# Kernel optimization log

Measured on AMD Instinct MI355X. Metric: run time of the kernel, lower is better.

## Reference

```python
import jax, jax.numpy as jnp
import numpy as np


def setup_inputs() -> dict:
    key = jax.random.key(0)
    k1, k2, k3, k4 = jax.random.split(key, 4)
    B, M, N = 8, 4096, 4096
    return {
        "pc_src": jax.random.normal(k1, (B, 3, M), dtype=jnp.float32),
        "pc_dst": jax.random.normal(k2, (B, 3, N), dtype=jnp.float32),
        "sigma_src": jax.random.uniform(k3, (B, M), dtype=jnp.float32),
        "sigma_dst": jax.random.uniform(k4, (B, N), dtype=jnp.float32),
    }


def reference(pc_src, pc_dst, sigma_src, sigma_dst):
    # Pairwise Euclidean distance: diff[b, m, n] = ||pc_src[b,:,m] - pc_dst[b,:,n]||_2
    d = pc_src[:, :, :, None] - pc_dst[:, :, None, :]  # [B, 3, M, N]
    diff = jnp.sqrt(jnp.sum(d * d, axis=1))            # [B, M, N]

    # src -> dst
    src_dst_min_dist = jnp.min(diff, axis=2)           # [B, M]
    src_dst_I = jnp.argmin(diff, axis=2)               # [B, M]
    selected_sigma_dst = jnp.take_along_axis(sigma_dst, src_dst_I, axis=1)
    sigma_src_dst = (sigma_src + selected_sigma_dst) / 2
    forward_loss = jnp.mean(src_dst_min_dist * sigma_src_dst)

    # dst -> src
    dst_src_min_dist = jnp.min(diff, axis=1)           # [B, N]
    dst_src_I = jnp.argmin(diff, axis=1)               # [B, N]
    selected_sigma_src = jnp.take_along_axis(sigma_src, dst_src_I, axis=1)
    sigma_dst_src = (sigma_dst + selected_sigma_src) / 2
    backward_loss = jnp.mean(dst_src_min_dist * sigma_dst_src)

    return forward_loss + backward_loss
```

## Files before the change

### kernel.cpp

```cpp
#include <hip/hip_runtime.h>
#include <math.h>
#include <cfloat>

#define BLOCK 256
#define QPT 8
#define CS  64

typedef float f32x2 __attribute__((ext_vector_type(2)));
typedef float f32x4 __attribute__((ext_vector_type(4)));
typedef unsigned long long u64;

__global__ __launch_bounds__(BLOCK, 4)
void chamfer_min_kernel(const float* __restrict__ pc_src,
                        const float* __restrict__ pc_dst,
                        u64* __restrict__ part,
                        int M, int N, int B, int Zn) {
    __shared__ f32x4 lds4[CS];

    const int b = blockIdx.y;
    const int z = blockIdx.z;
    const int dir = (z >= Zn) ? 1 : 0;
    const int chunk = dir ? (z - Zn) : z;

    const int NQ = dir ? N : M;
    const int NR = dir ? M : N;
    const float* pcq = dir ? pc_dst : pc_src;
    const float* pcr = dir ? pc_src : pc_dst;
    u64* pp = part + (dir ? (size_t)B * M : (size_t)0) + (size_t)b * NQ;

    const int n0 = chunk * CS;
    const int tid = threadIdx.x;

    const float* rbase = pcr + (size_t)b * 3 * NR + n0;
    if (tid < CS / 2) {
        const int p = tid;
        const f32x2 rx = *(const f32x2*)(rbase + 2 * p);
        const f32x2 ry = *(const f32x2*)(rbase + NR + 2 * p);
        const f32x2 rz = *(const f32x2*)(rbase + 2 * NR + 2 * p);
        f32x4 w0, w1;
        w0.x = -2.0f * rx.x; w0.y = -2.0f * rx.y;
        w0.z = -2.0f * ry.x; w0.w = -2.0f * ry.y;
        w1.x = -2.0f * rz.x; w1.y = -2.0f * rz.y;
        w1.z = fmaf(rx.x, rx.x, fmaf(ry.x, ry.x, rz.x * rz.x)) + 64.0f;
        w1.w = fmaf(rx.y, rx.y, fmaf(ry.y, ry.y, rz.y * rz.y)) + 64.0f;
        lds4[2 * p]     = w0;
        lds4[2 * p + 1] = w1;
    }

    const int q0 = blockIdx.x * (BLOCK * QPT) + tid;
    const float* qb = pcq + (size_t)b * 3 * NQ;
    float qx[QPT], qy[QPT], qz[QPT];
    unsigned kmin[QPT];
#pragma unroll
    for (int j = 0; j < QPT; ++j) {
        const int q = q0 + j * BLOCK;
        qx[j] = qb[q];
        qy[j] = qb[NQ + q];
        qz[j] = qb[2 * NQ + q];
        kmin[j] = 0xFFFFFFFFu;
    }

    __syncthreads();

    const unsigned mask = ~(unsigned)(CS - 1);
#pragma unroll
    for (int p = 0; p < CS / 2; ++p) {
        const f32x4 w0 = lds4[2 * p];
        const f32x4 w1 = lds4[2 * p + 1];
#pragma unroll
        for (int j = 0; j < QPT; ++j) {
            float e0, e1;
            asm("v_fma_f32 %1, %5, %10, %12\n\t"
                "v_fma_f32 %2, %5, %11, %13\n\t"
                "v_fma_f32 %1, %4, %8, %1\n\t"
                "v_fma_f32 %2, %4, %9, %2\n\t"
                "v_fma_f32 %1, %3, %6, %1\n\t"
                "v_fma_f32 %2, %3, %7, %2\n\t"
                "v_and_or_b32 %1, %1, %14, %15\n\t"
                "v_and_or_b32 %2, %2, %14, %16\n\t"
                "v_min3_u32 %0, %1, %2, %0"
                : "+v"(kmin[j]), "=&v"(e0), "=&v"(e1)
                : "v"(qx[j]), "v"(qy[j]), "v"(qz[j]),
                  "v"(w0.x), "v"(w0.y), "v"(w0.z), "v"(w0.w),
                  "v"(w1.x), "v"(w1.y), "v"(w1.z), "v"(w1.w),
                  "s"(mask), "i"(2 * p), "i"(2 * p + 1));
        }
    }

#pragma unroll
    for (int j = 0; j < QPT; ++j) {
        const int q = q0 + j * BLOCK;
        const unsigned gidx = (unsigned)n0 + (kmin[j] & (unsigned)(CS - 1));
        const u64 key = ((u64)(kmin[j] & mask) << 32) | (u64)gidx;
        atomicMin(&pp[q], key);
    }
}

__global__ void chamfer_reduce_kernel(const float* __restrict__ pc_src,
                                      const float* __restrict__ pc_dst,
                                      const float* __restrict__ sig_src,
                                      const float* __restrict__ sig_dst,
                                      const u64* __restrict__ part,
                                      float* __restrict__ out,
                                      int M, int N, int B) {
    __shared__ float red[BLOCK];
    const int TT = blockIdx.x * BLOCK + threadIdx.x;
    const int dir = (TT >= B * M);
    const int t = dir ? TT - B * M : TT;

    const int NQ = dir ? N : M;
    const int NR = dir ? M : N;
    const float* pcq  = dir ? pc_dst : pc_src;
    const float* pcr  = dir ? pc_src : pc_dst;
    const float* sigq = dir ? sig_dst : sig_src;
    const float* sigr = dir ? sig_src : sig_dst;
    const float scale = 1.0f / (float)(B * NQ);

    const int b = t / NQ;
    const int q = t - b * NQ;

    const int gidx = (int)(unsigned)part[TT];

    const float* qbase = pcq + (size_t)b * 3 * NQ;
    const float* rbase = pcr + (size_t)b * 3 * NR;
    const float dx = qbase[q]          - rbase[gidx];
    const float dy = qbase[NQ + q]     - rbase[NR + gidx];
    const float dz = qbase[2 * NQ + q] - rbase[2 * NR + gidx];
    const float dist = sqrtf(fmaf(dx, dx, fmaf(dy, dy, dz * dz)));

    const float s = 0.5f * (sigq[t] + sigr[(size_t)b * NR + gidx]);
    red[threadIdx.x] = dist * s * scale;
    __syncthreads();

    for (int w = BLOCK / 2; w > 0; w >>= 1) {
        if (threadIdx.x < w) red[threadIdx.x] += red[threadIdx.x + w];
        __syncthreads();
    }
    if (threadIdx.x == 0) atomicAdd(out, red[0]);
}

extern "C" void kernel_launch(void* const* d_in, const int* in_sizes, int n_in,
                              void* d_out, int out_size, void* d_ws, size_t ws_size,
                              hipStream_t stream) {
    const float* pc_src  = (const float*)d_in[0];
    const float* pc_dst  = (const float*)d_in[1];
    const float* sig_src = (const float*)d_in[2];
    const float* sig_dst = (const float*)d_in[3];
    float* out = (float*)d_out;

    const int B = 8;
    const int M = in_sizes[2] / B;
    const int N = in_sizes[3] / B;
    const int NMAX = (M > N) ? M : N;

    const int Zn = N / CS;
    const int Zm = M / CS;

    u64* part = (u64*)d_ws;
    const size_t partBytes = (size_t)B * (M + N) * sizeof(u64);

    hipMemsetAsync(part, 0xFF, partBytes, stream);
    hipMemsetAsync(d_out, 0, sizeof(float), stream);

    {
        dim3 grid(NMAX / (BLOCK * QPT), B, Zn + Zm);
        chamfer_min_kernel<<<grid, BLOCK, 0, stream>>>(
            pc_src, pc_dst, part, M, N, B, Zn);
    }
    {
        dim3 rgrid((B * (M + N)) / BLOCK);
        chamfer_reduce_kernel<<<rgrid, BLOCK, 0, stream>>>(
            pc_src, pc_dst, sig_src, sig_dst, part, out, M, N, B);
    }
}
```

Measured before the change: 49.55 us.

## Compute pairwise distance keys with fp16 MFMA and wave-shuffle argmin reduction

Replaces the VALU FMA distance loop with 32x32x16 fp16 MFMA tiles. Query coordinates form the A fragment, and -2x reference coordinates the B fragment. The accumulator is seeded with each reference point's squared norm plus an offset. Per-lane min keys pack the masked float bits with a tile index. A cross-lane shuffle reduction then recovers the column before the atomicMin. Reference chunks grow to 2048 points per block, and the reduce kernel masks the index. This cuts per-pair VALU work, but fp16 coordinates can change argmin picks on near-ties, and most of the MFMA K dimension is zero padding.

```diff
diff --git a/kernel.cpp b/kernel.cpp
--- a/kernel.cpp
+++ b/kernel.cpp
@@ -1,26 +1,39 @@
 #include <hip/hip_runtime.h>
 #include <math.h>
-#include <cfloat>
 
 #define BLOCK 256
-#define QPT 8
-#define CS  64
+#define CN    2048
+#define NT    (CN / 32)
 
-typedef float f32x2 __attribute__((ext_vector_type(2)));
-typedef float f32x4 __attribute__((ext_vector_type(4)));
+typedef _Float16 f16;
+typedef _Float16 f16x8 __attribute__((ext_vector_type(8)));
+typedef float f32x16 __attribute__((ext_vector_type(16)));
 typedef unsigned long long u64;
 
+union HU { f16 h; unsigned short u; };
+static __device__ __forceinline__ unsigned short h16(float x) {
+    HU v; v.h = (f16)x; return v.u;
+}
+static __device__ __forceinline__ u64 shflxor32_u64(u64 v, int m) {
+    unsigned lo = (unsigned)v, hi = (unsigned)(v >> 32);
+    lo = __shfl_xor(lo, m, 32);
+    hi = __shfl_xor(hi, m, 32);
+    return ((u64)hi << 32) | lo;
+}
+
 __global__ __launch_bounds__(BLOCK, 4)
-void chamfer_min_kernel(const float* __restrict__ pc_src,
-                        const float* __restrict__ pc_dst,
-                        u64* __restrict__ part,
-                        int M, int N, int B, int Zn) {
-    __shared__ f32x4 lds4[CS];
+void chamfer_mfma_kernel(const float* __restrict__ pc_src,
+                         const float* __restrict__ pc_dst,
+                         u64* __restrict__ part,
+                         int M, int N, int B, int Zc0) {
+    __shared__ uint4 lds_ref[CN + 1];
+    __shared__ float lds_w[CN];
 
-    const int b = blockIdx.y;
-    const int z = blockIdx.z;
-    const int dir = (z >= Zn) ? 1 : 0;
-    const int chunk = dir ? (z - Zn) : z;
+    const int rg = blockIdx.x;
+    const int b  = blockIdx.y;
+    const int z  = blockIdx.z;
+    const int dir = (z >= Zc0) ? 1 : 0;
+    const int chunk = dir ? (z - Zc0) : z;
 
     const int NQ = dir ? N : M;
     const int NR = dir ? M : N;
@@ -28,71 +41,72 @@
     const float* pcr = dir ? pc_src : pc_dst;
     u64* pp = part + (dir ? (size_t)B * M : (size_t)0) + (size_t)b * NQ;
 
-    const int n0 = chunk * CS;
     const int tid = threadIdx.x;
+    const int lane = tid & 63;
+    const int wid = tid >> 6;
+    const int n0 = chunk * CN;
 
-    const float* rbase = pcr + (size_t)b * 3 * NR + n0;
-    if (tid < CS / 2) {
-        const int p = tid;
-        const f32x2 rx = *(const f32x2*)(rbase + 2 * p);
-        const f32x2 ry = *(const f32x2*)(rbase + NR + 2 * p);
-        const f32x2 rz = *(const f32x2*)(rbase + 2 * NR + 2 * p);
-        f32x4 w0, w1;
-        w0.x = -2.0f * rx.x; w0.y = -2.0f * rx.y;
-        w0.z = -2.0f * ry.x; w0.w = -2.0f * ry.y;
-        w1.x = -2.0f * rz.x; w1.y = -2.0f * rz.y;
-        w1.z = fmaf(rx.x, rx.x, fmaf(ry.x, ry.x, rz.x * rz.x)) + 64.0f;
-        w1.w = fmaf(rx.y, rx.y, fmaf(ry.y, ry.y, rz.y * rz.y)) + 64.0f;
-        lds4[2 * p]     = w0;
-        lds4[2 * p + 1] = w1;
+    const float* rb = pcr + (size_t)b * 3 * NR + n0;
+    for (int i = tid; i < CN; i += BLOCK) {
+        const float rx = rb[i], ry = rb[NR + i], rz = rb[2 * NR + i];
+        const unsigned u0 = (unsigned)h16(-2.0f * rx) | ((unsigned)h16(-2.0f * ry) << 16);
+        const unsigned u1 = (unsigned)h16(-2.0f * rz);
+        lds_ref[i] = make_uint4(u0, u1, 0u, 0u);
+        lds_w[i] = fmaf(rx, rx, fmaf(ry, ry, rz * rz)) + 64.0f;
     }
+    if (tid == 0) lds_ref[CN] = make_uint4(0u, 0u, 0u, 0u);
 
-    const int q0 = blockIdx.x * (BLOCK * QPT) + tid;
-    const float* qb = pcq + (size_t)b * 3 * NQ;
-    float qx[QPT], qy[QPT], qz[QPT];
-    unsigned kmin[QPT];
-#pragma unroll
-    for (int j = 0; j < QPT; ++j) {
-        const int q = q0 + j * BLOCK;
-        qx[j] = qb[q];
-        qy[j] = qb[NQ + q];
-        qz[j] = qb[2 * NQ + q];
-        kmin[j] = 0xFFFFFFFFu;
+    const int row0 = rg * 128 + wid * 32;
+    f16x8 afrag = {0, 0, 0, 0, 0, 0, 0, 0};
+    if (lane < 32) {
+        const float* qb = pcq + (size_t)b * 3 * NQ + row0 + lane;
+        afrag[0] = (f16)qb[0];
+        afrag[1] = (f16)qb[NQ];
+        afrag[2] = (f16)qb[2 * NQ];
     }
 
     __syncthreads();
 
-    const unsigned mask = ~(unsigned)(CS - 1);
+    const int col = lane & 31;
+    const bool lo = (lane < 32);
+    const uint4* bptr = lo ? &lds_ref[col] : &lds_ref[CN];
+    const int bstep = lo ? 32 : 0;
+
+    unsigned kmin[16];
 #pragma unroll
-    for (int p = 0; p < CS / 2; ++p) {
-        const f32x4 w0 = lds4[2 * p];
-        const f32x4 w1 = lds4[2 * p + 1];
+    for (int r = 0; r < 16; ++r) kmin[r] = 0xFFFFFFFFu;
+
+    const unsigned emask = ~127u;
+    const unsigned tj0 = (unsigned)(chunk * NT);
+
+    for (int t = 0; t < NT; ++t) {
+        const f16x8 bfrag = *(const f16x8*)bptr;
+        bptr += bstep;
+        const float wval = lds_w[t * 32 + col];
+        f32x16 acc;
 #pragma unroll
-        for (int j = 0; j < QPT; ++j) {
-            float e0, e1;
-            asm("v_fma_f32 %1, %5, %10, %12\n\t"
-                "v_fma_f32 %2, %5, %11, %13\n\t"
-                "v_fma_f32 %1, %4, %8, %1\n\t"
-                "v_fma_f32 %2, %4, %9, %2\n\t"
-                "v_fma_f32 %1, %3, %6, %1\n\t"
-                "v_fma_f32 %2, %3, %7, %2\n\t"
-                "v_and_or_b32 %1, %1, %14, %15\n\t"
-                "v_and_or_b32 %2, %2, %14, %16\n\t"
-                "v_min3_u32 %0, %1, %2, %0"
-                : "+v"(kmin[j]), "=&v"(e0), "=&v"(e1)
-                : "v"(qx[j]), "v"(qy[j]), "v"(qz[j]),
-                  "v"(w0.x), "v"(w0.y), "v"(w0.z), "v"(w0.w),
-                  "v"(w1.x), "v"(w1.y), "v"(w1.z), "v"(w1.w),
-                  "s"(mask), "i"(2 * p), "i"(2 * p + 1));
+        for (int r = 0; r < 16; ++r) acc[r] = wval;
+        acc = __builtin_amdgcn_mfma_f32_32x32x16_f16(afrag, bfrag, acc, 0, 0, 0);
+        const unsigned tj = tj0 + (unsigned)t;
+#pragma unroll
+        for (int r = 0; r < 16; ++r) {
+            const unsigned key = (__float_as_uint(acc[r]) & emask) | tj;
+            kmin[r] = key < kmin[r] ? key : kmin[r];
         }
     }
 
+    const int rhalf = (lane >> 5) * 4;
 #pragma unroll
-    for (int j = 0; j < QPT; ++j) {
-        const int q = q0 + j * BLOCK;
-        const unsigned gidx = (unsigned)n0 + (kmin[j] & (unsigned)(CS - 1));
-        const u64 key = ((u64)(kmin[j] & mask) << 32) | (u64)gidx;
-        atomicMin(&pp[q], key);
+    for (int r = 0; r < 16; ++r) {
+        u64 k64 = ((u64)kmin[r] << 5) | (unsigned)col;
+        for (int m2 = 1; m2 <= 16; m2 <<= 1) {
+            const u64 o = shflxor32_u64(k64, m2);
+            k64 = (o < k64) ? o : k64;
+        }
+        if (col == 0) {
+            const int row = (r & 3) + 8 * (r >> 2) + rhalf;
+            atomicMin(&pp[row0 + row], k64);
+        }
     }
 }
 
@@ -119,7 +133,7 @@
     const int b = t / NQ;
     const int q = t - b * NQ;
 
-    const int gidx = (int)(unsigned)part[TT];
+    const int gidx = (int)((unsigned)part[TT] & (unsigned)(NR - 1));
 
     const float* qbase = pcq + (size_t)b * 3 * NQ;
     const float* rbase = pcr + (size_t)b * 3 * NR;
@@ -151,10 +165,6 @@
     const int B = 8;
     const int M = in_sizes[2] / B;
     const int N = in_sizes[3] / B;
-    const int NMAX = (M > N) ? M : N;
-
-    const int Zn = N / CS;
-    const int Zm = M / CS;
 
     u64* part = (u64*)d_ws;
     const size_t partBytes = (size_t)B * (M + N) * sizeof(u64);
@@ -162,10 +172,13 @@
     hipMemsetAsync(part, 0xFF, partBytes, stream);
     hipMemsetAsync(d_out, 0, sizeof(float), stream);
 
+    const int Zc0 = N / CN;
+    const int Zc1 = M / CN;
+
     {
-        dim3 grid(NMAX / (BLOCK * QPT), B, Zn + Zm);
-        chamfer_min_kernel<<<grid, BLOCK, 0, stream>>>(
-            pc_src, pc_dst, part, M, N, B, Zn);
+        dim3 grid(M / 128, B, Zc0 + Zc1);
+        chamfer_mfma_kernel<<<grid, BLOCK, 0, stream>>>(
+            pc_src, pc_dst, part, M, N, B, Zc0);
     }
     {
         dim3 rgrid((B * (M + N)) / BLOCK);
```

Result: slower. 56.87 us (+14.8%).

## Precompute packed reference points in setup kernel and read them directly from global

Applied to the files above, without the earlier changes.

Adds a setup kernel that packs each reference point into a uint4 (-2x, -2y, -2z, |r|^2+64), initializes the partial-min buffer, and zeroes the output, replacing the two memsets. The min kernel drops its LDS staging and barrier, reads the packed points straight from global memory (uniform, so cached), and swaps the inline asm for plain C key/min code. It also raises launch bounds to 8 waves. The aim is less per-block setup and sync overhead plus higher occupancy. The risks are one extra launch, and compiler code that may be less tight than the hand-written min3/and_or sequence.

```diff
diff --git a/kernel.cpp b/kernel.cpp
--- a/kernel.cpp
+++ b/kernel.cpp
@@ -1,54 +1,59 @@
 #include <hip/hip_runtime.h>
 #include <math.h>
-#include <cfloat>
 
 #define BLOCK 256
 #define QPT 8
 #define CS  64
 
-typedef float f32x2 __attribute__((ext_vector_type(2)));
-typedef float f32x4 __attribute__((ext_vector_type(4)));
 typedef unsigned long long u64;
 
-__global__ __launch_bounds__(BLOCK, 4)
-void chamfer_min_kernel(const float* __restrict__ pc_src,
+__global__ void chamfer_setup_kernel(const float* __restrict__ pc_src,
+                                     const float* __restrict__ pc_dst,
+                                     uint4* __restrict__ packed,
+                                     u64* __restrict__ part,
+                                     float* __restrict__ out,
+                                     int M, int N, int B) {
+    const int t = blockIdx.x * BLOCK + threadIdx.x;
+    const int TOT0 = B * N;
+    const int dir = (t >= TOT0);
+    const int NR = dir ? M : N;
+    const float* pc = dir ? pc_src : pc_dst;
+    const int tt = dir ? t - TOT0 : t;
+    const int b = tt / NR, i = tt - b * NR;
+    const float* rb = pc + (size_t)b * 3 * NR;
+    const float rx = rb[i], ry = rb[NR + i], rz = rb[2 * NR + i];
+    uint4 v;
+    v.x = __float_as_uint(-2.0f * rx);
+    v.y = __float_as_uint(-2.0f * ry);
+    v.z = __float_as_uint(-2.0f * rz);
+    v.w = __float_as_uint(fmaf(rx, rx, fmaf(ry, ry, rz * rz)) + 64.0f);
+    packed[t] = v;
+    part[t] = ~0ull;
+    if (t == 0) *out = 0.0f;
+}
+
+__global__ __launch_bounds__(BLOCK, 8)
+void chamfer_min_kernel(const uint4* __restrict__ packed,
+                        const float* __restrict__ pc_src,
                         const float* __restrict__ pc_dst,
                         u64* __restrict__ part,
-                        int M, int N, int B, int Zn) {
-    __shared__ f32x4 lds4[CS];
-
+                        int M, int N, int B, int Zc0) {
     const int b = blockIdx.y;
     const int z = blockIdx.z;
-    const int dir = (z >= Zn) ? 1 : 0;
-    const int chunk = dir ? (z - Zn) : z;
+    const int dir = (z >= Zc0) ? 1 : 0;
+    const int chunk = dir ? (z - Zc0) : z;
 
     const int NQ = dir ? N : M;
-    const int NR = dir ? M : N;
     const float* pcq = dir ? pc_dst : pc_src;
-    const float* pcr = dir ? pc_src : pc_dst;
+    const uint4* rp = packed
+        + (dir ? (size_t)B * N + (size_t)b * M : (size_t)b * N)
+        + (size_t)chunk * CS;
     u64* pp = part + (dir ? (size_t)B * M : (size_t)0) + (size_t)b * NQ;
 
-    const int n0 = chunk * CS;
     const int tid = threadIdx.x;
-
-    const float* rbase = pcr + (size_t)b * 3 * NR + n0;
-    if (tid < CS / 2) {
-        const int p = tid;
-        const f32x2 rx = *(const f32x2*)(rbase + 2 * p);
-        const f32x2 ry = *(const f32x2*)(rbase + NR + 2 * p);
-        const f32x2 rz = *(const f32x2*)(rbase + 2 * NR + 2 * p);
-        f32x4 w0, w1;
-        w0.x = -2.0f * rx.x; w0.y = -2.0f * rx.y;
-        w0.z = -2.0f * ry.x; w0.w = -2.0f * ry.y;
-        w1.x = -2.0f * rz.x; w1.y = -2.0f * rz.y;
-        w1.z = fmaf(rx.x, rx.x, fmaf(ry.x, ry.x, rz.x * rz.x)) + 64.0f;
-        w1.w = fmaf(rx.y, rx.y, fmaf(ry.y, ry.y, rz.y * rz.y)) + 64.0f;
-        lds4[2 * p]     = w0;
-        lds4[2 * p + 1] = w1;
-    }
-
     const int q0 = blockIdx.x * (BLOCK * QPT) + tid;
     const float* qb = pcq + (size_t)b * 3 * NQ;
+
     float qx[QPT], qy[QPT], qz[QPT];
     unsigned kmin[QPT];
 #pragma unroll
@@ -60,38 +65,27 @@
         kmin[j] = 0xFFFFFFFFu;
     }
 
-    __syncthreads();
-
-    const unsigned mask = ~(unsigned)(CS - 1);
-#pragma unroll
-    for (int p = 0; p < CS / 2; ++p) {
-        const f32x4 w0 = lds4[2 * p];
-        const f32x4 w1 = lds4[2 * p + 1];
+#pragma unroll 8
+    for (int i = 0; i < CS; ++i) {
+        const uint4 rv = rp[i];
+        const float rx = __uint_as_float(rv.x);
+        const float ry = __uint_as_float(rv.y);
+        const float rz = __uint_as_float(rv.z);
+        const float wv = __uint_as_float(rv.w);
+        const unsigned idx = (unsigned)i;
 #pragma unroll
         for (int j = 0; j < QPT; ++j) {
-            float e0, e1;
-            asm("v_fma_f32 %1, %5, %10, %12\n\t"
-                "v_fma_f32 %2, %5, %11, %13\n\t"
-                "v_fma_f32 %1, %4, %8, %1\n\t"
-                "v_fma_f32 %2, %4, %9, %2\n\t"
-                "v_fma_f32 %1, %3, %6, %1\n\t"
-                "v_fma_f32 %2, %3, %7, %2\n\t"
-                "v_and_or_b32 %1, %1, %14, %15\n\t"
-                "v_and_or_b32 %2, %2, %14, %16\n\t"
-                "v_min3_u32 %0, %1, %2, %0"
-                : "+v"(kmin[j]), "=&v"(e0), "=&v"(e1)
-                : "v"(qx[j]), "v"(qy[j]), "v"(qz[j]),
-                  "v"(w0.x), "v"(w0.y), "v"(w0.z), "v"(w0.w),
-                  "v"(w1.x), "v"(w1.y), "v"(w1.z), "v"(w1.w),
-                  "s"(mask), "i"(2 * p), "i"(2 * p + 1));
+            const float e = fmaf(qx[j], rx, fmaf(qy[j], ry, fmaf(qz[j], rz, wv)));
+            const unsigned key = (__float_as_uint(e) & ~63u) | idx;
+            kmin[j] = key < kmin[j] ? key : kmin[j];
         }
     }
 
+    const unsigned n0 = (unsigned)(chunk * CS);
 #pragma unroll
     for (int j = 0; j < QPT; ++j) {
         const int q = q0 + j * BLOCK;
-        const unsigned gidx = (unsigned)n0 + (kmin[j] & (unsigned)(CS - 1));
-        const u64 key = ((u64)(kmin[j] & mask) << 32) | (u64)gidx;
+        const u64 key = ((u64)(kmin[j] & ~63u) << 32) | (u64)(n0 + (kmin[j] & 63u));
         atomicMin(&pp[q], key);
     }
 }
@@ -151,24 +145,25 @@
     const int B = 8;
     const int M = in_sizes[2] / B;
     const int N = in_sizes[3] / B;
-    const int NMAX = (M > N) ? M : N;
-
-    const int Zn = N / CS;
-    const int Zm = M / CS;
 
     u64* part = (u64*)d_ws;
-    const size_t partBytes = (size_t)B * (M + N) * sizeof(u64);
+    uint4* packed = (uint4*)((char*)d_ws + (size_t)B * (M + N) * sizeof(u64));
 
-    hipMemsetAsync(part, 0xFF, partBytes, stream);
-    hipMemsetAsync(d_out, 0, sizeof(float), stream);
+    const int TOT = B * (M + N);
 
     {
-        dim3 grid(NMAX / (BLOCK * QPT), B, Zn + Zm);
-        chamfer_min_kernel<<<grid, BLOCK, 0, stream>>>(
-            pc_src, pc_dst, part, M, N, B, Zn);
+        chamfer_setup_kernel<<<TOT / BLOCK, BLOCK, 0, stream>>>(
+            pc_src, pc_dst, packed, part, out, M, N, B);
     }
     {
-        dim3 rgrid((B * (M + N)) / BLOCK);
+        const int Zc0 = N / CS;
+        const int Zc1 = M / CS;
+        dim3 grid(M / (BLOCK * QPT), B, Zc0 + Zc1);
+        chamfer_min_kernel<<<grid, BLOCK, 0, stream>>>(
+            packed, pc_src, pc_dst, part, M, N, B, Zc0);
+    }
+    {
+        dim3 rgrid(TOT / BLOCK);
         chamfer_reduce_kernel<<<rgrid, BLOCK, 0, stream>>>(
             pc_src, pc_dst, sig_src, sig_dst, part, out, M, N, B);
     }
```

Result: no change. 49.74 us (+0.4%).
